# Kernel tuning notes

Hardware: AMD Instinct MI355X
Metric: run time of the kernel (lower is better)

The kernel has to match this reference:

```python
import jax, jax.numpy as jnp
import numpy as np

B, L, D, Y = 8, 2500, 512, 8921


def setup_inputs() -> dict:
    key = jax.random.key(0)
    k1, k2, k3, k4, k5 = jax.random.split(key, 5)
    x = jax.random.normal(k1, (B, L, D), dtype=jnp.float32)
    target = jax.random.uniform(k2, (B, Y), dtype=jnp.float32)
    U_w = jax.random.normal(k3, (Y, D), dtype=jnp.float32) * (1.0 / np.sqrt(D))
    final_w = jax.random.normal(k4, (Y, D), dtype=jnp.float32) * (1.0 / np.sqrt(D))
    final_b = jax.random.normal(k5, (Y,), dtype=jnp.float32) * 0.01
    return {"x": x, "target": target, "text_inputs": 0,
            "U_w": U_w, "final_w": final_w, "final_b": final_b}


def _bce_with_logits(y, t):
    # stable mean BCE-with-logits, matching torch BCEWithLogitsLoss (reduction='mean')
    return jnp.mean(jnp.maximum(y, 0.0) - y * t + jnp.log1p(jnp.exp(-jnp.abs(y))))


def reference(x, target, text_inputs, U_w, final_w, final_b):
    # label-wise attention scores: [B, Y, L]
    scores = jnp.einsum('yd,bld->byl', U_w, x)
    alpha = jax.nn.softmax(scores, axis=-1)
    # attended context per label: [B, Y, D]
    m = jnp.einsum('byl,bld->byd', alpha, x)
    # per-label dot-product readout: [B, Y]
    y = jnp.einsum('yd,byd->by', final_w, m) + final_b
    loss = _bce_with_logits(y, target)
    return (y, loss)
```

## Files before the change

### kernel.cpp

```cpp
#include <hip/hip_runtime.h>
#include <math.h>

#define B_  8
#define L_  2500
#define D_  512
#define Y_  8921
#define LP  2560
#define YP  8960

#define WS_F16_HALVES  (B_ * LP * D_ + 2 * YP * D_)
#define ACC_FLOATS     (2 * B_ * YP)

typedef _Float16 f16x8 __attribute__((ext_vector_type(8)));
typedef float    f32x4 __attribute__((ext_vector_type(4)));

__device__ __forceinline__ void load_lds16(const _Float16* g, _Float16* l) {
  __builtin_amdgcn_global_load_lds(
      (const __attribute__((address_space(1))) unsigned int*)g,
      (__attribute__((address_space(3))) unsigned int*)l, 16, 0, 0);
}

__global__ void k_convert(const float* __restrict__ x,
                          const float* __restrict__ Uw,
                          const float* __restrict__ Fw,
                          _Float16* __restrict__ ws,
                          float* __restrict__ loss_slot) {
  if (blockIdx.x == 0 && threadIdx.x == 0) *loss_slot = 0.0f;
  const int NX = B_ * LP * (D_ / 8);
  int idx = blockIdx.x * 256 + threadIdx.x;
  if (idx < ACC_FLOATS) ((float*)(ws + WS_F16_HALVES))[idx] = 0.0f;
  const float* src = nullptr;
  if (idx < NX) {
    int b  = idx / (LP * 64);
    int r  = idx - b * (LP * 64);
    int l  = r >> 6;
    int d8 = r & 63;
    if (l < L_) src = x + (((long)b * L_ + l) * D_ + d8 * 8);
  } else {
    int u = idx - NX;
    int r = u >> 6;
    int d8 = u & 63;
    int group = r >> 4, sub = r & 15;
    int y = group * 8 + (sub & 7);
    if (y < Y_) src = (sub < 8 ? Uw : Fw) + (long)y * D_ + d8 * 8;
  }
  f16x8 o;
  if (src) {
    const float4* s4 = (const float4*)src;
    float4 a = s4[0], c = s4[1];
    o[0] = (_Float16)a.x; o[1] = (_Float16)a.y; o[2] = (_Float16)a.z; o[3] = (_Float16)a.w;
    o[4] = (_Float16)c.x; o[5] = (_Float16)c.y; o[6] = (_Float16)c.z; o[7] = (_Float16)c.w;
  } else {
    for (int i = 0; i < 8; ++i) o[i] = (_Float16)0.0f;
  }
  ((f16x8*)ws)[idx] = o;
}

__global__ __launch_bounds__(256, 2)
void k_attn(const _Float16* __restrict__ ws,
            float* __restrict__ accG) {
  __shared__ __align__(16) _Float16 TILE[24576];
  _Float16* GT = TILE;
  _Float16* XT = TILE + 8192;

  const int tid  = threadIdx.x;
  const int lane = tid & 63;
  const int wave = tid >> 6;
  const int wy = wave & 1;
  const int wl = wave >> 1;
  const int yt = blockIdx.x;
  const int b  = blockIdx.y;
  const int lh = blockIdx.z;

  const _Float16* Xg = ws + (long)b * LP * D_ + (long)lh * (LP / 2) * D_;
  const _Float16* Gg = ws + (long)B_ * LP * D_ + (long)yt * 128 * D_;

  const int srow = lane >> 3;
  const int sg8  = ((lane & 7) ^ srow) * 8;
  const _Float16* gsrc[12];
  _Float16*       gdst[12];
  #pragma unroll
  for (int i = 0; i < 12; ++i) {
    int seg = wave * 12 + i;
    const _Float16* base;
    int r;
    if (seg < 16) { base = Gg; r = seg * 8; }
    else          { base = Xg; r = (seg - 16) * 8; }
    gsrc[i] = base + (long)(r + srow) * D_ + sg8;
    gdst[i] = TILE + seg * 512;
  }

  const int arow = wy * 64 + (lane & 15);
  const int xrow = wl * 128 + (lane & 15);
  const int r7   = lane & 7;
  const int gb   = lane >> 4;
  const bool sLow = (lane < 32);

  float redP[4][4];
  #pragma unroll
  for (int i = 0; i < 4; ++i)
    for (int v = 0; v < 4; ++v) redP[i][v] = 0.0f;

  for (int lt = 0; lt < 5; ++lt) {
    f32x4 acc[4][8];
    #pragma unroll
    for (int mi = 0; mi < 4; ++mi)
      for (int ni = 0; ni < 8; ++ni) {
        f32x4 z = {0.0f, 0.0f, 0.0f, 0.0f};
        acc[mi][ni] = z;
      }
    const long xofs = (long)lt * 256 * D_;
    for (int kk = 0; kk < D_; kk += 64) {
      __syncthreads();
      #pragma unroll
      for (int i = 0; i < 12; ++i) {
        const _Float16* s = gsrc[i] + kk;
        if (wave * 12 + i >= 16) s += xofs;
        load_lds16(s, gdst[i]);
      }
      __syncthreads();
      #pragma unroll
      for (int ks = 0; ks < 2; ++ks) {
        int off = (((ks * 4 + gb) ^ r7) * 8);
        f16x8 bx[8];
        #pragma unroll
        for (int ni = 0; ni < 8; ++ni)
          bx[ni] = *(const f16x8*)&XT[(xrow + ni * 16) * 64 + off];
        #pragma unroll
        for (int mi = 0; mi < 4; ++mi) {
          f16x8 a = *(const f16x8*)&GT[(arow + mi * 16) * 64 + off];
          #pragma unroll
          for (int ni = 0; ni < 8; ++ni)
            acc[mi][ni] = __builtin_amdgcn_mfma_f32_16x16x32_f16(a, bx[ni], acc[mi][ni], 0, 0, 0);
        }
      }
    }
    #pragma unroll
    for (int mi = 0; mi < 4; ++mi)
      for (int ni = 0; ni < 8; ++ni)
        #pragma unroll
        for (int v = 0; v < 4; ++v) {
          float a = acc[mi][ni][v];
          float e = __expf(a);
          float p = __shfl_xor(e, 32, 64);
          redP[mi][v] += sLow ? e : p * a;
        }
  }

  for (int m = 1; m < 16; m <<= 1)
    #pragma unroll
    for (int mi = 0; mi < 4; ++mi)
      for (int v = 0; v < 4; ++v)
        redP[mi][v] += __shfl_xor(redP[mi][v], m, 64);
  if ((lane & 15) == 0) {
    float* dst = accG + (sLow ? 0 : B_ * YP);
    #pragma unroll
    for (int mi = 0; mi < 4; ++mi)
      for (int v = 0; v < 4; ++v) {
        int y = yt * 64 + wy * 32 + mi * 8 + ((lane >> 4) & 1) * 4 + v;
        atomicAdd(&dst[b * YP + y], redP[mi][v]);
      }
  }
}

__global__ void k_final(const float* __restrict__ accG,
                        const float* __restrict__ fb,
                        float* __restrict__ out) {
  int id = blockIdx.x * 256 + threadIdx.x;
  if (id >= B_ * Y_) return;
  int b = id / Y_, y = id - b * Y_;
  float den = accG[b * YP + y] - (float)(LP - L_);
  out[id] = accG[B_ * YP + b * YP + y] / den + fb[y];
}

__global__ void k_loss(const float* __restrict__ y,
                       const float* __restrict__ t,
                       float* __restrict__ loss) {
  float p = 0.0f;
  for (int i = blockIdx.x * 256 + threadIdx.x; i < B_ * Y_; i += gridDim.x * 256) {
    float v = y[i], tg = t[i];
    p += fmaxf(v, 0.0f) - v * tg + log1pf(__expf(-fabsf(v)));
  }
  for (int m = 32; m; m >>= 1) p += __shfl_down(p, m, 64);
  __shared__ float wsum[4];
  int lane = threadIdx.x & 63, wv = threadIdx.x >> 6;
  if (lane == 0) wsum[wv] = p;
  __syncthreads();
  if (threadIdx.x == 0) {
    float s = wsum[0] + wsum[1] + wsum[2] + wsum[3];
    atomicAdd(loss, s * (1.0f / (float)(B_ * Y_)));
  }
}

extern "C" void kernel_launch(void* const* d_in, const int* in_sizes, int n_in,
                              void* d_out, int out_size, void* d_ws, size_t ws_size,
                              hipStream_t stream) {
  (void)in_sizes; (void)n_in; (void)out_size; (void)ws_size;
  const float* x       = (const float*)d_in[0];
  const float* target  = (const float*)d_in[1];
  const float* U_w     = (const float*)d_in[3];
  const float* final_w = (const float*)d_in[4];
  const float* final_b = (const float*)d_in[5];
  float* out = (float*)d_out;
  _Float16* ws = (_Float16*)d_ws;
  float* accG = (float*)(ws + WS_F16_HALVES);

  k_convert<<<9600, 256, 0, stream>>>(x, U_w, final_w, ws, out + B_ * Y_);

  dim3 g(YP / 64, B_, 2);
  k_attn<<<g, 256, 0, stream>>>(ws, accG);

  k_final<<<(B_ * Y_ + 255) / 256, 256, 0, stream>>>(accG, final_b, out);
  k_loss<<<140, 256, 0, stream>>>(out, target, out + B_ * Y_);
}
```

Baseline: 560.5 us.

## Pre-swizzle label weights into MFMA fragment order and load A operands directly from global

After: 516.1 us. 7.9% less time.

```diff
diff --git a/kernel.cpp b/kernel.cpp
--- a/kernel.cpp
+++ b/kernel.cpp
@@ -37,12 +37,16 @@
     int d8 = r & 63;
     if (l < L_) src = x + (((long)b * L_ + l) * D_ + d8 * 8);
   } else {
-    int u = idx - NX;
-    int r = u >> 6;
-    int d8 = u & 63;
-    int group = r >> 4, sub = r & 15;
-    int y = group * 8 + (sub & 7);
-    if (y < Y_) src = (sub < 8 ? Uw : Fw) + (long)y * D_ + d8 * 8;
+    int u    = idx - NX;
+    int lane = u & 63;
+    int mi   = (u >> 6) & 7;
+    int kk2  = (u >> 9) & 15;
+    int yt   = u >> 13;
+    int grow = yt * 128 + mi * 16 + (lane & 15);
+    int sub  = grow & 15;
+    int y    = (grow >> 4) * 8 + (sub & 7);
+    int k8   = kk2 * 4 + (lane >> 4);
+    if (y < Y_) src = (sub < 8 ? Uw : Fw) + (long)y * D_ + k8 * 8;
   }
   f16x8 o;
   if (src) {
@@ -59,9 +63,7 @@
 __global__ __launch_bounds__(256, 2)
 void k_attn(const _Float16* __restrict__ ws,
             float* __restrict__ accG) {
-  __shared__ __align__(16) _Float16 TILE[24576];
-  _Float16* GT = TILE;
-  _Float16* XT = TILE + 8192;
+  __shared__ __align__(16) _Float16 XT[16384];
 
   const int tid  = threadIdx.x;
   const int lane = tid & 63;
@@ -73,24 +75,20 @@
   const int lh = blockIdx.z;
 
   const _Float16* Xg = ws + (long)b * LP * D_ + (long)lh * (LP / 2) * D_;
-  const _Float16* Gg = ws + (long)B_ * LP * D_ + (long)yt * 128 * D_;
+  const _Float16* Ga = ws + (long)B_ * LP * D_ + (long)yt * (128 * 512)
+                          + (wy * 4) * 512 + lane * 8;
 
   const int srow = lane >> 3;
   const int sg8  = ((lane & 7) ^ srow) * 8;
-  const _Float16* gsrc[12];
-  _Float16*       gdst[12];
+  const _Float16* xsrc[8];
+  _Float16*       xdst[8];
   #pragma unroll
-  for (int i = 0; i < 12; ++i) {
-    int seg = wave * 12 + i;
-    const _Float16* base;
-    int r;
-    if (seg < 16) { base = Gg; r = seg * 8; }
-    else          { base = Xg; r = (seg - 16) * 8; }
-    gsrc[i] = base + (long)(r + srow) * D_ + sg8;
-    gdst[i] = TILE + seg * 512;
-  }
-
-  const int arow = wy * 64 + (lane & 15);
+  for (int i = 0; i < 8; ++i) {
+    int seg = wave * 8 + i;
+    xsrc[i] = Xg + (long)(seg * 8 + srow) * D_ + sg8;
+    xdst[i] = XT + seg * 512;
+  }
+
   const int xrow = wl * 128 + (lane & 15);
   const int r7   = lane & 7;
   const int gb   = lane >> 4;
@@ -110,14 +108,17 @@
         acc[mi][ni] = z;
       }
     const long xofs = (long)lt * 256 * D_;
-    for (int kk = 0; kk < D_; kk += 64) {
+    for (int kkstep = 0; kkstep < 8; ++kkstep) {
+      f16x8 au[2][4];
+      #pragma unroll
+      for (int ks = 0; ks < 2; ++ks)
+        #pragma unroll
+        for (int mi = 0; mi < 4; ++mi)
+          au[ks][mi] = *(const f16x8*)(Ga + (size_t)(kkstep * 2 + ks) * 4096 + mi * 512);
       __syncthreads();
       #pragma unroll
-      for (int i = 0; i < 12; ++i) {
-        const _Float16* s = gsrc[i] + kk;
-        if (wave * 12 + i >= 16) s += xofs;
-        load_lds16(s, gdst[i]);
-      }
+      for (int i = 0; i < 8; ++i)
+        load_lds16(xsrc[i] + xofs + kkstep * 64, xdst[i]);
       __syncthreads();
       #pragma unroll
       for (int ks = 0; ks < 2; ++ks) {
@@ -127,12 +128,10 @@
         for (int ni = 0; ni < 8; ++ni)
           bx[ni] = *(const f16x8*)&XT[(xrow + ni * 16) * 64 + off];
         #pragma unroll
-        for (int mi = 0; mi < 4; ++mi) {
-          f16x8 a = *(const f16x8*)&GT[(arow + mi * 16) * 64 + off];
+        for (int mi = 0; mi < 4; ++mi)
           #pragma unroll
           for (int ni = 0; ni < 8; ++ni)
-            acc[mi][ni] = __builtin_amdgcn_mfma_f32_16x16x32_f16(a, bx[ni], acc[mi][ni], 0, 0, 0);
-        }
+            acc[mi][ni] = __builtin_amdgcn_mfma_f32_16x16x32_f16(au[ks][mi], bx[ni], acc[mi][ni], 0, 0, 0);
       }
     }
     #pragma unroll
```
